# Optimization experiments

Hardware: AMD Instinct MI355X
Metric: run time of the kernel (lower is better)

## Reference

```python
import jax, jax.numpy as jnp
import numpy as np

N = 50000
E = 100000
H = 768          # hidden_size
NH = 12          # num_heads
HD = H // NH     # head dim = 64
NG = 64          # number of graphs in batch
NC = 10          # num_classes
NEG_SLOPE = 0.2


def _p(key, shape, scale=0.05):
    return jax.random.normal(key, shape, dtype=jnp.float32) * scale


def setup_inputs() -> dict:
    key = jax.random.key(0)
    ks = jax.random.split(key, 24)
    x = jax.random.normal(ks[0], (N, 3), dtype=jnp.float32)
    edge_index = jax.random.randint(ks[1], (2, E), 0, N, dtype=jnp.int32)
    batch = jnp.sort(jax.random.randint(ks[2], (N,), 0, NG, dtype=jnp.int32))
    inp = {
        'x': x, 'edge_index': edge_index, 'batch': batch,
        # GCN layers
        'w1': _p(ks[3], (3, H)), 'b1': jnp.zeros((H,), jnp.float32),
        'w2': _p(ks[4], (H, H)), 'b2': jnp.zeros((H,), jnp.float32),
        'w3': _p(ks[5], (H, H)), 'b3': jnp.zeros((H,), jnp.float32),
        # GAT layer 1
        'wg1': _p(ks[6], (H, H)), 'as1': _p(ks[7], (NH, HD)), 'ad1': _p(ks[8], (NH, HD)), 'bg1': jnp.zeros((H,), jnp.float32),
        # GAT layer 2
        'wg2': _p(ks[9], (H, H)), 'as2': _p(ks[10], (NH, HD)), 'ad2': _p(ks[11], (NH, HD)), 'bg2': jnp.zeros((H,), jnp.float32),
        # classifier MLP
        'wc1': _p(ks[12], (H, H // 2)), 'bc1': jnp.zeros((H // 2,), jnp.float32),
        'wc2': _p(ks[13], (H // 2, NC)), 'bc2': jnp.zeros((NC,), jnp.float32),
    }
    return inp


def _add_self_loops(edge_index):
    loop = jnp.arange(N, dtype=edge_index.dtype)
    src = jnp.concatenate([edge_index[0], loop])
    dst = jnp.concatenate([edge_index[1], loop])
    return src, dst


def gcn_conv(x, w, b, src, dst):
    # PyG GCNConv: self-loops + symmetric normalization D^-1/2 A D^-1/2
    h = x @ w                                   # [N, out]
    deg = jnp.zeros((N,), h.dtype).at[dst].add(1.0)   # includes self-loops -> >= 1
    dinv = jax.lax.rsqrt(deg)
    norm = (dinv[src] * dinv[dst])[:, None]     # [E', 1]
    msg = h[src] * norm                          # gather-scale
    out = jnp.zeros_like(h).at[dst].add(msg)     # scatter-add
    return out + b


def gat_conv(x, w, a_src, a_dst, b, src, dst):
    # PyG GATConv: self-loops, LeakyReLU(0.2), scatter-softmax over dst, concat heads
    h = (x @ w).reshape(N, NH, HD)
    alpha_s = jnp.einsum('nhd,hd->nh', h, a_src)  # [N, H]
    alpha_d = jnp.einsum('nhd,hd->nh', h, a_dst)
    e = jax.nn.leaky_relu(alpha_s[src] + alpha_d[dst], NEG_SLOPE)  # [E', H]
    m = jax.ops.segment_max(e, dst, num_segments=N)                 # [N, H]
    ex = jnp.exp(e - m[dst])
    s = jax.ops.segment_sum(ex, dst, num_segments=N)
    alpha = ex / s[dst]                                             # [E', H]
    out = jax.ops.segment_sum(h[src] * alpha[:, :, None], dst, num_segments=N)
    return out.reshape(N, NH * HD) + b


def global_mean_pool(x, batch):
    s = jax.ops.segment_sum(x, batch, num_segments=NG)
    cnt = jax.ops.segment_sum(jnp.ones((N,), x.dtype), batch, num_segments=NG)
    return s / jnp.maximum(cnt, 1.0)[:, None]


def reference(x, edge_index, batch, w1, b1, w2, b2, w3, b3,
              wg1, as1, ad1, bg1, wg2, as2, ad2, bg2,
              wc1, bc1, wc2, bc2):
    src, dst = _add_self_loops(edge_index)
    h = jax.nn.relu(gcn_conv(x, w1, b1, src, dst))
    # dropout is identity in eval mode
    h = jax.nn.relu(gcn_conv(h, w2, b2, src, dst))
    h = jax.nn.relu(gcn_conv(h, w3, b3, src, dst))
    h = jax.nn.relu(gat_conv(h, wg1, as1, ad1, bg1, src, dst))
    h = gat_conv(h, wg2, as2, ad2, bg2, src, dst)
    g = global_mean_pool(h, batch)                 # [NG, H]
    z = jax.nn.relu(g @ wc1 + bc1)
    logits = z @ wc2 + bc2                         # [NG, NC]
    return logits
```

## Files before the change

### kernel.cpp

```cpp
#include <hip/hip_runtime.h>
#include <math.h>

#define N_NODES 50000
#define N_EDGES 100000
#define H 768
#define NH 12
#define HD 64
#define NG 64
#define NC 10
#define H2 384
#define PCH 32
#define NSB 196

typedef _Float16 h8  __attribute__((ext_vector_type(8)));
typedef _Float16 h4v __attribute__((ext_vector_type(4)));
typedef float    ffrag __attribute__((ext_vector_type(4)));

__device__ _Float16 g_ah[(size_t)N_NODES * H];
__device__ _Float16 g_ch[(size_t)N_NODES * H];
__device__ _Float16 g_wh[4 * H * H];
__device__ float    g_dinv[N_NODES];
__device__ int      g_degi[N_NODES];
__device__ int      g_bsum[256];
__device__ int      g_boff[256];
__device__ int      g_cursor[N_NODES];
__device__ int      g_rowptr[N_NODES + 1];
__device__ int      g_csrsrc[N_EDGES];
__device__ float    g_aS[(size_t)N_NODES * NH];
__device__ float    g_aD[(size_t)N_NODES * NH];
__device__ float    g_ppool[(size_t)NG * PCH * H];

__device__ inline int clampi(int v, int hi) { return (v < 0) ? 0 : (v >= hi ? hi - 1 : v); }

__device__ inline void gload_lds16(const _Float16* g, _Float16* s) {
    __builtin_amdgcn_global_load_lds(
        (const __attribute__((address_space(1))) void*)g,
        (__attribute__((address_space(3))) void*)s, 16, 0, 0);
}

__global__ void fill_i32(int* p, int n, int v) {
    int i = blockIdx.x * blockDim.x + threadIdx.x;
    if (i < n) p[i] = v;
}

__global__ void count_deg(const int* __restrict__ dst, int* __restrict__ degi) {
    int e = blockIdx.x * blockDim.x + threadIdx.x;
    if (e < N_EDGES) atomicAdd(&degi[clampi(dst[e], N_NODES)], 1);
}

__global__ __launch_bounds__(256) void scan1(const int* __restrict__ degi, int* __restrict__ bsum) {
    __shared__ int s[256];
    int b = blockIdx.x, t = threadIdx.x;
    int idx = b * 256 + t;
    s[t] = (idx < N_NODES) ? degi[idx] : 0;
    __syncthreads();
    for (int off = 128; off > 0; off >>= 1) {
        if (t < off) s[t] += s[t + off];
        __syncthreads();
    }
    if (t == 0) bsum[b] = s[0];
}

__global__ __launch_bounds__(256) void scan2(const int* __restrict__ bsum, int* __restrict__ boff,
                                             int* __restrict__ rowptr) {
    __shared__ int s[256];
    int t = threadIdx.x;
    int v = (t < NSB) ? bsum[t] : 0;
    s[t] = v;
    __syncthreads();
    for (int off = 1; off < 256; off <<= 1) {
        int x = (t >= off) ? s[t - off] : 0;
        __syncthreads();
        s[t] += x;
        __syncthreads();
    }
    if (t < NSB) boff[t] = s[t] - v;
    if (t == NSB - 1) rowptr[N_NODES] = s[t];
}

__global__ __launch_bounds__(256) void scan3(const int* __restrict__ degi, const int* __restrict__ boff,
                                             int* __restrict__ rowptr, int* __restrict__ cursor,
                                             float* __restrict__ dinv) {
    __shared__ int s[256];
    int b = blockIdx.x, t = threadIdx.x;
    int idx = b * 256 + t;
    int v = (idx < N_NODES) ? degi[idx] : 0;
    s[t] = v;
    __syncthreads();
    for (int off = 1; off < 256; off <<= 1) {
        int x = (t >= off) ? s[t - off] : 0;
        __syncthreads();
        s[t] += x;
        __syncthreads();
    }
    if (idx < N_NODES) {
        int excl = s[t] - v + boff[b];
        rowptr[idx] = excl;
        cursor[idx] = excl;
        dinv[idx] = rsqrtf((float)v + 1.0f);
    }
}

__global__ void bin_edges(const int* __restrict__ src, const int* __restrict__ dst,
                          int* __restrict__ cursor, int* __restrict__ csrsrc) {
    int e = blockIdx.x * blockDim.x + threadIdx.x;
    if (e >= N_EDGES) return;
    int d = clampi(dst[e], N_NODES);
    int pos = atomicAdd(&cursor[d], 1);
    if (pos >= 0 && pos < N_EDGES) csrsrc[pos] = clampi(src[e], N_NODES);
}

__global__ void split_wT4(const float* __restrict__ w2, const float* __restrict__ w3,
                          const float* __restrict__ wg1, const float* __restrict__ wg2,
                          _Float16* __restrict__ out) {
    int idx = blockIdx.x * blockDim.x + threadIdx.x;
    if (idx >= 4 * H * H) return;
    int l = idx / (H * H), r = idx % (H * H);
    const float* w = (l == 0) ? w2 : (l == 1) ? w3 : (l == 2) ? wg1 : wg2;
    int n = r % H, k = r / H;
    out[(size_t)l * H * H + (size_t)n * H + k] = (_Float16)w[(size_t)k * H + n];
}

__global__ void gcn1_fused(const int* __restrict__ rowptr, const int* __restrict__ csrsrc,
                           const float* __restrict__ x, const float* __restrict__ dinv,
                           const float* __restrict__ w1, const float* __restrict__ b1,
                           _Float16* __restrict__ hi) {
    int d = blockIdx.x * 2 + (threadIdx.x / 96);
    int t = threadIdx.x % 96;
    if (d >= N_NODES) return;
    float dd = dinv[d];
    float c = dd * dd;
    float s0 = x[d*3] * c, s1 = x[d*3+1] * c, s2 = x[d*3+2] * c;
    int beg = rowptr[d], end = rowptr[d + 1];
    for (int i = beg; i < end; i++) {
        int s = csrsrc[i];
        float cc = dinv[s] * dd;
        s0 += x[s*3] * cc; s1 += x[s*3+1] * cc; s2 += x[s*3+2] * cc;
    }
    int j0 = t * 8;
    h8 o;
    #pragma unroll
    for (int k = 0; k < 8; k++) {
        int j = j0 + k;
        float v = s0 * w1[j] + s1 * w1[H + j] + s2 * w1[2*H + j] + b1[j];
        o[k] = (_Float16)fmaxf(v, 0.f);
    }
    ((h8*)(hi + (size_t)d * H))[t] = o;
}

__global__ __launch_bounds__(512) void gemm_f16(const _Float16* __restrict__ a,
                                                const _Float16* __restrict__ bt,
                                                _Float16* __restrict__ C, int M,
                                                const float* __restrict__ asf,
                                                const float* __restrict__ adf,
                                                float* __restrict__ aS,
                                                float* __restrict__ aD) {
    __shared__ _Float16 sA[2][128 * 32], sB[2][128 * 32];
    int tid = threadIdx.x;
    int wave = tid >> 6, lane = tid & 63;
    int quad = lane >> 4, l16 = lane & 15;

    int id = blockIdx.x;
    int x = id & 7;
    int s = id >> 3;
    int strip = x + 8 * (s / 6);
    int colt = s % 6;
    if (strip >= (N_NODES + 127) / 128) return;
    int row0 = strip * 128, col0 = colt * 128;
    int wr = (wave >> 1) * 32, wc = (wave & 1) * 64;

    int rr = lane >> 2;
    int kc = (((lane & 3) ^ ((lane >> 3) & 3)) << 3);
    const _Float16* gptr[2];
    int sel[2];
    int soff[2];
    #pragma unroll
    for (int k = 0; k < 2; k++) {
        int sg = wave * 2 + k;
        int isA = (sg < 8);
        int rowgroup = sg & 7;
        int r = (isA ? row0 : col0) + rowgroup * 16 + rr;
        if (isA && r >= M) r = M - 1;
        gptr[k] = (isA ? a : bt) + (size_t)r * H + kc;
        sel[k] = isA ? 0 : 1;
        soff[k] = rowgroup * 512;
    }

    int fsw = (quad ^ ((l16 >> 1) & 3)) * 8;

    ffrag acc[2][4];
    #pragma unroll
    for (int i = 0; i < 2; i++)
        #pragma unroll
        for (int j = 0; j < 4; j++) { ffrag z = {0.f, 0.f, 0.f, 0.f}; acc[i][j] = z; }

    #pragma unroll
    for (int k = 0; k < 2; k++)
        gload_lds16(gptr[k], (sel[k] ? &sB[0][0] : &sA[0][0]) + soff[k]);

    #pragma unroll 1
    for (int kt = 0; kt < H / 32; kt++) {
        int cur = kt & 1;
        __syncthreads();
        if (kt + 1 < H / 32) {
            int koff = (kt + 1) * 32;
            #pragma unroll
            for (int k = 0; k < 2; k++)
                gload_lds16(gptr[k] + koff,
                            (sel[k] ? &sB[cur ^ 1][0] : &sA[cur ^ 1][0]) + soff[k]);
        }

        const _Float16* pA = sA[cur];
        const _Float16* pB = sB[cur];
        h8 fa[2], fb[4];
        #pragma unroll
        for (int i = 0; i < 2; i++)
            fa[i] = *reinterpret_cast<const h8*>(&pA[(wr + i * 16 + l16) * 32 + fsw]);
        #pragma unroll
        for (int j = 0; j < 4; j++)
            fb[j] = *reinterpret_cast<const h8*>(&pB[(wc + j * 16 + l16) * 32 + fsw]);
        #pragma unroll
        for (int i = 0; i < 2; i++)
            #pragma unroll
            for (int j = 0; j < 4; j++)
                acc[i][j] = __builtin_amdgcn_mfma_f32_16x16x32_f16(fa[i], fb[j], acc[i][j], 0, 0, 0);
    }

    #pragma unroll
    for (int i = 0; i < 2; i++)
        #pragma unroll
        for (int r = 0; r < 4; r++) {
            int row = row0 + wr + i * 16 + quad * 4 + r;
            if (row >= M) continue;
            #pragma unroll
            for (int j = 0; j < 4; j++)
                C[(size_t)row * H + col0 + wc + j * 16 + l16] = (_Float16)acc[i][j][r];
        }

    if (asf) {
        int head = (col0 + wc) >> 6;
        float as_c[4], ad_c[4];
        #pragma unroll
        for (int j = 0; j < 4; j++) {
            int col = col0 + wc + j * 16 + l16;
            as_c[j] = asf[col];
            ad_c[j] = adf[col];
        }
        #pragma unroll
        for (int i = 0; i < 2; i++)
            #pragma unroll
            for (int r = 0; r < 4; r++) {
                float ps = 0.f, pd = 0.f;
                #pragma unroll
                for (int j = 0; j < 4; j++) {
                    ps += acc[i][j][r] * as_c[j];
                    pd += acc[i][j][r] * ad_c[j];
                }
                ps += __shfl_xor(ps, 1);  pd += __shfl_xor(pd, 1);
                ps += __shfl_xor(ps, 2);  pd += __shfl_xor(pd, 2);
                ps += __shfl_xor(ps, 4);  pd += __shfl_xor(pd, 4);
                ps += __shfl_xor(ps, 8);  pd += __shfl_xor(pd, 8);
                int row = row0 + wr + i * 16 + quad * 4 + r;
                if (l16 == 0 && row < M) {
                    aS[row * NH + head] = ps;
                    aD[row * NH + head] = pd;
                }
            }
    }
}

__global__ void gcn_gather(const int* __restrict__ rowptr, const int* __restrict__ csrsrc,
                           const _Float16* __restrict__ h, const float* __restrict__ dinv,
                           const float* __restrict__ bias, _Float16* __restrict__ hi) {
    int d = blockIdx.x * 2 + (threadIdx.x / 96);
    int t = threadIdx.x % 96;
    if (d >= N_NODES) return;
    float dd = dinv[d];
    float c = dd * dd;
    h8 v = ((const h8*)(h + (size_t)d * H))[t];
    float acc[8];
    #pragma unroll
    for (int k = 0; k < 8; k++) acc[k] = (float)v[k] * c;
    int beg = rowptr[d], end = rowptr[d + 1];
    for (int i = beg; i < end; i++) {
        int s = csrsrc[i];
        float cc = dinv[s] * dd;
        h8 u = ((const h8*)(h + (size_t)s * H))[t];
        #pragma unroll
        for (int k = 0; k < 8; k++) acc[k] += (float)u[k] * cc;
    }
    float4 b0 = ((const float4*)bias)[2 * t];
    float4 b1 = ((const float4*)bias)[2 * t + 1];
    h8 o;
    o[0] = (_Float16)fmaxf(acc[0] + b0.x, 0.f);
    o[1] = (_Float16)fmaxf(acc[1] + b0.y, 0.f);
    o[2] = (_Float16)fmaxf(acc[2] + b0.z, 0.f);
    o[3] = (_Float16)fmaxf(acc[3] + b0.w, 0.f);
    o[4] = (_Float16)fmaxf(acc[4] + b1.x, 0.f);
    o[5] = (_Float16)fmaxf(acc[5] + b1.y, 0.f);
    o[6] = (_Float16)fmaxf(acc[6] + b1.z, 0.f);
    o[7] = (_Float16)fmaxf(acc[7] + b1.w, 0.f);
    ((h8*)(hi + (size_t)d * H))[t] = o;
}

__device__ inline float lrelu(float v) { return (v > 0.f) ? v : 0.2f * v; }

__global__ void gat_gather(const int* __restrict__ rowptr, const int* __restrict__ csrsrc,
                           const _Float16* __restrict__ h, const float* __restrict__ aS,
                           const float* __restrict__ aD, const float* __restrict__ bias,
                           _Float16* __restrict__ hi, int relu) {
    int d = blockIdx.x * 2 + (threadIdx.x / 96);
    int t = threadIdx.x % 96;
    if (d >= N_NODES) return;
    int hh = t >> 3;
    int beg = rowptr[d], end = rowptr[d + 1];
    float adv = aD[d * NH + hh];
    float eself = lrelu(aS[d * NH + hh] + adv);
    float m = eself;
    for (int i = beg; i < end; i++)
        m = fmaxf(m, lrelu(aS[csrsrc[i] * NH + hh] + adv));
    float ssum = __expf(eself - m);
    for (int i = beg; i < end; i++)
        ssum += __expf(lrelu(aS[csrsrc[i] * NH + hh] + adv) - m);
    float inv = 1.0f / ssum;
    float cself = __expf(eself - m) * inv;
    h8 v = ((const h8*)(h + (size_t)d * H))[t];
    float acc[8];
    #pragma unroll
    for (int k = 0; k < 8; k++) acc[k] = (float)v[k] * cself;
    for (int i = beg; i < end; i++) {
        int s = csrsrc[i];
        float c = __expf(lrelu(aS[s * NH + hh] + adv) - m) * inv;
        h8 u = ((const h8*)(h + (size_t)s * H))[t];
        #pragma unroll
        for (int k = 0; k < 8; k++) acc[k] += (float)u[k] * c;
    }
    float4 b0 = ((const float4*)bias)[2 * t];
    float4 b1 = ((const float4*)bias)[2 * t + 1];
    acc[0] += b0.x; acc[1] += b0.y; acc[2] += b0.z; acc[3] += b0.w;
    acc[4] += b1.x; acc[5] += b1.y; acc[6] += b1.z; acc[7] += b1.w;
    if (relu) {
        #pragma unroll
        for (int k = 0; k < 8; k++) acc[k] = fmaxf(acc[k], 0.f);
    }
    h8 o;
    #pragma unroll
    for (int k = 0; k < 8; k++) o[k] = (_Float16)acc[k];
    ((h8*)(hi + (size_t)d * H))[t] = o;
}

__device__ inline int lower_bound_i(const int* b, int n, int key) {
    int lo = 0, hi = n;
    while (lo < hi) { int mid = (lo + hi) >> 1; if (b[mid] < key) lo = mid + 1; else hi = mid; }
    return lo;
}

__global__ void pool_partial(const int* __restrict__ batch, const _Float16* __restrict__ h,
                             float* __restrict__ ppool) {
    int g = blockIdx.x / PCH, c = blockIdx.x % PCH;
    int t = threadIdx.x;
    int lo = lower_bound_i(batch, N_NODES, g);
    int hi = lower_bound_i(batch, N_NODES, g + 1);
    int len = hi - lo;
    int chunk = (len + PCH - 1) / PCH;
    int s = lo + c * chunk;
    int e = s + chunk; if (e > hi) e = hi;
    float4 a = {0, 0, 0, 0};
    for (int n = s; n < e; n++) {
        h4v v = ((const h4v*)(h + (size_t)n * H))[t];
        a.x += (float)v[0]; a.y += (float)v[1]; a.z += (float)v[2]; a.w += (float)v[3];
    }
    ((float4*)(ppool + (size_t)blockIdx.x * H))[t] = a;
}

__global__ __launch_bounds__(384) void pool_mlp(const int* __restrict__ batch,
                                                const float* __restrict__ ppool,
                                                const float* __restrict__ wc1,
                                                const float* __restrict__ bc1,
                                                const float* __restrict__ wc2,
                                                const float* __restrict__ bc2,
                                                float* __restrict__ out) {
    __shared__ float row[H];
    __shared__ float z[H2];
    int g = blockIdx.x, t = threadIdx.x;
    int lo = lower_bound_i(batch, N_NODES, g);
    int hi = lower_bound_i(batch, N_NODES, g + 1);
    float inv = 1.0f / fmaxf((float)(hi - lo), 1.0f);
    for (int c0 = t; c0 < H; c0 += 384) {
        float a = 0.f;
        for (int c = 0; c < PCH; c++) a += ppool[(size_t)(g * PCH + c) * H + c0];
        row[c0] = a * inv;
    }
    __syncthreads();
    float acc = bc1[t];
    for (int k = 0; k < H; k++) acc += row[k] * wc1[(size_t)k * H2 + t];
    z[t] = fmaxf(acc, 0.f);
    __syncthreads();
    if (t < NC) {
        float l = bc2[t];
        for (int k = 0; k < H2; k++) l += z[k] * wc2[(size_t)k * NC + t];
        out[g * NC + t] = l;
    }
}

extern "C" void kernel_launch(void* const* d_in, const int* in_sizes, int n_in,
                              void* d_out, int out_size, void* d_ws, size_t ws_size,
                              hipStream_t stream) {
    (void)d_ws; (void)ws_size;
    const float* x     = (const float*)d_in[0];
    const int*   ei    = (const int*)d_in[1];
    const int*   batch = (const int*)d_in[2];
    const float* w1  = (const float*)d_in[3];  const float* b1  = (const float*)d_in[4];
    const float* w2  = (const float*)d_in[5];  const float* b2  = (const float*)d_in[6];
    const float* w3  = (const float*)d_in[7];  const float* b3  = (const float*)d_in[8];
    const float* wg1 = (const float*)d_in[9];  const float* as1 = (const float*)d_in[10];
    const float* ad1 = (const float*)d_in[11]; const float* bg1 = (const float*)d_in[12];
    const float* wg2 = (const float*)d_in[13]; const float* as2 = (const float*)d_in[14];
    const float* ad2 = (const float*)d_in[15]; const float* bg2 = (const float*)d_in[16];
    const float* wc1 = (const float*)d_in[17]; const float* bc1 = (const float*)d_in[18];
    const float* wc2 = (const float*)d_in[19]; const float* bc2 = (const float*)d_in[20];

    const int* srcp = ei;
    const int* dstp = ei + N_EDGES;

    float *dinv, *aS, *aD, *ppool;
    _Float16 *ah, *ch, *wh;
    int *degi, *bsum, *boff, *cursor, *rowptr, *csrsrc;
    hipGetSymbolAddress((void**)&ah,     HIP_SYMBOL(g_ah));
    hipGetSymbolAddress((void**)&ch,     HIP_SYMBOL(g_ch));
    hipGetSymbolAddress((void**)&wh,     HIP_SYMBOL(g_wh));
    hipGetSymbolAddress((void**)&dinv,   HIP_SYMBOL(g_dinv));
    hipGetSymbolAddress((void**)&degi,   HIP_SYMBOL(g_degi));
    hipGetSymbolAddress((void**)&bsum,   HIP_SYMBOL(g_bsum));
    hipGetSymbolAddress((void**)&boff,   HIP_SYMBOL(g_boff));
    hipGetSymbolAddress((void**)&cursor, HIP_SYMBOL(g_cursor));
    hipGetSymbolAddress((void**)&rowptr, HIP_SYMBOL(g_rowptr));
    hipGetSymbolAddress((void**)&csrsrc, HIP_SYMBOL(g_csrsrc));
    hipGetSymbolAddress((void**)&aS,     HIP_SYMBOL(g_aS));
    hipGetSymbolAddress((void**)&aD,     HIP_SYMBOL(g_aD));
    hipGetSymbolAddress((void**)&ppool,  HIP_SYMBOL(g_ppool));

    auto cdiv = [](int a, int b) { return (a + b - 1) / b; };
    int ggrid = 8 * cdiv(cdiv(N_NODES, 128), 8) * (H / 128);
    int ngath = cdiv(N_NODES, 2);
    size_t HH = (size_t)H * H;

    split_wT4<<<cdiv(4*H*H,256),256,0,stream>>>(w2, w3, wg1, wg2, wh);

    fill_i32<<<cdiv(N_NODES,256),256,0,stream>>>(degi, N_NODES, 0);
    count_deg<<<cdiv(N_EDGES,256),256,0,stream>>>(dstp, degi);
    scan1<<<NSB,256,0,stream>>>(degi, bsum);
    scan2<<<1,256,0,stream>>>(bsum, boff, rowptr);
    scan3<<<NSB,256,0,stream>>>(degi, boff, rowptr, cursor, dinv);
    bin_edges<<<cdiv(N_EDGES,256),256,0,stream>>>(srcp, dstp, cursor, csrsrc);

    gcn1_fused<<<ngath,192,0,stream>>>(rowptr, csrsrc, x, dinv, w1, b1, ah);

    gemm_f16<<<ggrid,512,0,stream>>>(ah, wh + 0*HH, ch, N_NODES,
                                     (const float*)nullptr, (const float*)nullptr,
                                     (float*)nullptr, (float*)nullptr);
    gcn_gather<<<ngath,192,0,stream>>>(rowptr, csrsrc, ch, dinv, b2, ah);

    gemm_f16<<<ggrid,512,0,stream>>>(ah, wh + 1*HH, ch, N_NODES,
                                     (const float*)nullptr, (const float*)nullptr,
                                     (float*)nullptr, (float*)nullptr);
    gcn_gather<<<ngath,192,0,stream>>>(rowptr, csrsrc, ch, dinv, b3, ah);

    gemm_f16<<<ggrid,512,0,stream>>>(ah, wh + 2*HH, ch, N_NODES, as1, ad1, aS, aD);
    gat_gather<<<ngath,192,0,stream>>>(rowptr, csrsrc, ch, aS, aD, bg1, ah, 1);

    gemm_f16<<<ggrid,512,0,stream>>>(ah, wh + 3*HH, ch, N_NODES, as2, ad2, aS, aD);
    gat_gather<<<ngath,192,0,stream>>>(rowptr, csrsrc, ch, aS, aD, bg2, ah, 0);

    pool_partial<<<NG*PCH,192,0,stream>>>(batch, ah, ppool);
    pool_mlp<<<NG,384,0,stream>>>(batch, ppool, wc1, bc1, wc2, bc2, (float*)d_out);
}
```

Before: 913.1 us.

## Enlarge GEMM tile to 256x128 with triple-buffered LDS pipeline

Restructures the f16 MFMA GEMM so each block computes a 256x128 tile instead of 128x128, and each wave a 64x64 sub-tile, to raise reuse per LDS load. The LDS buffering goes from double to triple, with two K-slices prefetched ahead, explicit vmcnt waits and a single barrier per iteration. It also raises priority around the MFMA block and remaps block IDs across XCDs. In exchange it uses more registers for the accumulators, needs a larger LDS footprint that limits occupancy, and launches fewer blocks (196x6 grid).

```diff
diff --git a/kernel.cpp b/kernel.cpp
--- a/kernel.cpp
+++ b/kernel.cpp
@@ -148,86 +148,95 @@
     ((h8*)(hi + (size_t)d * H))[t] = o;
 }
 
-__global__ __launch_bounds__(512) void gemm_f16(const _Float16* __restrict__ a,
-                                                const _Float16* __restrict__ bt,
-                                                _Float16* __restrict__ C, int M,
-                                                const float* __restrict__ asf,
-                                                const float* __restrict__ adf,
-                                                float* __restrict__ aS,
-                                                float* __restrict__ aD) {
-    __shared__ _Float16 sA[2][128 * 32], sB[2][128 * 32];
+__global__ __launch_bounds__(512, 2) void gemm_f16(const _Float16* __restrict__ a,
+                                                   const _Float16* __restrict__ bt,
+                                                   _Float16* __restrict__ C, int M,
+                                                   const float* __restrict__ asf,
+                                                   const float* __restrict__ adf,
+                                                   float* __restrict__ aS,
+                                                   float* __restrict__ aD) {
+    __shared__ alignas(16) _Float16 lds[3][12288];
+
     int tid = threadIdx.x;
     int wave = tid >> 6, lane = tid & 63;
     int quad = lane >> 4, l16 = lane & 15;
-
-    int id = blockIdx.x;
-    int x = id & 7;
-    int s = id >> 3;
-    int strip = x + 8 * (s / 6);
-    int colt = s % 6;
-    if (strip >= (N_NODES + 127) / 128) return;
-    int row0 = strip * 128, col0 = colt * 128;
-    int wr = (wave >> 1) * 32, wc = (wave & 1) * 64;
+    int wr = (wave >> 1) * 64, wc = (wave & 1) * 64;
+
+    int orig = blockIdx.x;
+    int wgid = (orig & 7) * 147 + (orig >> 3);
+    int strip = wgid / 6, colt = wgid % 6;
+    int row0 = strip * 256, col0 = colt * 128;
 
     int rr = lane >> 2;
-    int kc = (((lane & 3) ^ ((lane >> 3) & 3)) << 3);
-    const _Float16* gptr[2];
-    int sel[2];
-    int soff[2];
-    #pragma unroll
-    for (int k = 0; k < 2; k++) {
-        int sg = wave * 2 + k;
-        int isA = (sg < 8);
-        int rowgroup = sg & 7;
-        int r = (isA ? row0 : col0) + rowgroup * 16 + rr;
+    int kc = ((lane & 3) ^ ((lane >> 3) & 3)) << 3;
+    const _Float16* gptr[3];
+    int soff[3];
+    #pragma unroll
+    for (int k = 0; k < 3; k++) {
+        int u = wave * 3 + k;
+        int isA = (u < 16);
+        int rg = isA ? u : (u - 16);
+        int r = (isA ? row0 : col0) + rg * 16 + rr;
         if (isA && r >= M) r = M - 1;
         gptr[k] = (isA ? a : bt) + (size_t)r * H + kc;
-        sel[k] = isA ? 0 : 1;
-        soff[k] = rowgroup * 512;
+        soff[k] = (isA ? 0 : 8192) + rg * 512;
     }
 
     int fsw = (quad ^ ((l16 >> 1) & 3)) * 8;
 
-    ffrag acc[2][4];
-    #pragma unroll
-    for (int i = 0; i < 2; i++)
+    ffrag acc[4][4];
+    #pragma unroll
+    for (int i = 0; i < 4; i++)
         #pragma unroll
         for (int j = 0; j < 4; j++) { ffrag z = {0.f, 0.f, 0.f, 0.f}; acc[i][j] = z; }
 
-    #pragma unroll
-    for (int k = 0; k < 2; k++)
-        gload_lds16(gptr[k], (sel[k] ? &sB[0][0] : &sA[0][0]) + soff[k]);
+    _Float16* p0 = &lds[0][0];
+    _Float16* p1 = &lds[1][0];
+    _Float16* p2 = &lds[2][0];
+
+    #pragma unroll
+    for (int k = 0; k < 3; k++) gload_lds16(gptr[k],      p0 + soff[k]);
+    #pragma unroll
+    for (int k = 0; k < 3; k++) gload_lds16(gptr[k] + 32, p1 + soff[k]);
+    asm volatile("s_waitcnt vmcnt(3)" ::: "memory");
+    __builtin_amdgcn_s_barrier();
+
+    _Float16 *pc = p0, *pn = p1, *ps = p2;
 
     #pragma unroll 1
-    for (int kt = 0; kt < H / 32; kt++) {
-        int cur = kt & 1;
-        __syncthreads();
-        if (kt + 1 < H / 32) {
-            int koff = (kt + 1) * 32;
+    for (int kt = 0; kt < 24; kt++) {
+        if (kt <= 21) {
+            int koff = (kt + 2) * 32;
             #pragma unroll
-            for (int k = 0; k < 2; k++)
-                gload_lds16(gptr[k] + koff,
-                            (sel[k] ? &sB[cur ^ 1][0] : &sA[cur ^ 1][0]) + soff[k]);
+            for (int k = 0; k < 3; k++) gload_lds16(gptr[k] + koff, ps + soff[k]);
         }
-
-        const _Float16* pA = sA[cur];
-        const _Float16* pB = sB[cur];
-        h8 fa[2], fb[4];
-        #pragma unroll
-        for (int i = 0; i < 2; i++)
-            fa[i] = *reinterpret_cast<const h8*>(&pA[(wr + i * 16 + l16) * 32 + fsw]);
+        h8 fa[4], fb[4];
+        #pragma unroll
+        for (int i = 0; i < 4; i++)
+            fa[i] = *reinterpret_cast<const h8*>(pc + (wr + i * 16 + l16) * 32 + fsw);
         #pragma unroll
         for (int j = 0; j < 4; j++)
-            fb[j] = *reinterpret_cast<const h8*>(&pB[(wc + j * 16 + l16) * 32 + fsw]);
-        #pragma unroll
-        for (int i = 0; i < 2; i++)
+            fb[j] = *reinterpret_cast<const h8*>(pc + 8192 + (wc + j * 16 + l16) * 32 + fsw);
+        asm volatile("s_waitcnt lgkmcnt(0)" ::: "memory");
+        __builtin_amdgcn_sched_barrier(0);
+        __builtin_amdgcn_s_setprio(1);
+        #pragma unroll
+        for (int i = 0; i < 4; i++)
             #pragma unroll
             for (int j = 0; j < 4; j++)
                 acc[i][j] = __builtin_amdgcn_mfma_f32_16x16x32_f16(fa[i], fb[j], acc[i][j], 0, 0, 0);
-    }
-
-    #pragma unroll
-    for (int i = 0; i < 2; i++)
+        __builtin_amdgcn_s_setprio(0);
+        if (kt <= 21)      asm volatile("s_waitcnt vmcnt(3)" ::: "memory");
+        else if (kt == 22) asm volatile("s_waitcnt vmcnt(0)" ::: "memory");
+        if (kt <= 22) {
+            __builtin_amdgcn_sched_barrier(0);
+            __builtin_amdgcn_s_barrier();
+        }
+        _Float16* t = pc; pc = pn; pn = ps; ps = t;
+    }
+
+    #pragma unroll
+    for (int i = 0; i < 4; i++)
         #pragma unroll
         for (int r = 0; r < 4; r++) {
             int row = row0 + wr + i * 16 + quad * 4 + r;
@@ -247,22 +256,22 @@
             ad_c[j] = adf[col];
         }
         #pragma unroll
-        for (int i = 0; i < 2; i++)
+        for (int i = 0; i < 4; i++)
             #pragma unroll
             for (int r = 0; r < 4; r++) {
-                float ps = 0.f, pd = 0.f;
+                float ps2 = 0.f, pd = 0.f;
                 #pragma unroll
                 for (int j = 0; j < 4; j++) {
-                    ps += acc[i][j][r] * as_c[j];
-                    pd += acc[i][j][r] * ad_c[j];
+                    ps2 += acc[i][j][r] * as_c[j];
+                    pd  += acc[i][j][r] * ad_c[j];
                 }
-                ps += __shfl_xor(ps, 1);  pd += __shfl_xor(pd, 1);
-                ps += __shfl_xor(ps, 2);  pd += __shfl_xor(pd, 2);
-                ps += __shfl_xor(ps, 4);  pd += __shfl_xor(pd, 4);
-                ps += __shfl_xor(ps, 8);  pd += __shfl_xor(pd, 8);
+                ps2 += __shfl_xor(ps2, 1);  pd += __shfl_xor(pd, 1);
+                ps2 += __shfl_xor(ps2, 2);  pd += __shfl_xor(pd, 2);
+                ps2 += __shfl_xor(ps2, 4);  pd += __shfl_xor(pd, 4);
+                ps2 += __shfl_xor(ps2, 8);  pd += __shfl_xor(pd, 8);
                 int row = row0 + wr + i * 16 + quad * 4 + r;
                 if (l16 == 0 && row < M) {
-                    aS[row * NH + head] = ps;
+                    aS[row * NH + head] = ps2;
                     aD[row * NH + head] = pd;
                 }
             }
@@ -441,7 +450,7 @@
     hipGetSymbolAddress((void**)&ppool,  HIP_SYMBOL(g_ppool));
 
     auto cdiv = [](int a, int b) { return (a + b - 1) / b; };
-    int ggrid = 8 * cdiv(cdiv(N_NODES, 128), 8) * (H / 128);
+    int ggrid = cdiv(N_NODES, 256) * (H / 128);
     int ngath = cdiv(N_NODES, 2);
     size_t HH = (size_t)H * H;
 
```

Measured after the change: 840.5 us. -8.0%, faster.
